# Kernel tuning notes

Measured on AMD Instinct MI355X. Metric: run time of the kernel, lower is better.

The kernel has to match this reference:

```python
import jax, jax.numpy as jnp
import numpy as np

EMBED_DIM = 1024
NUM_HEADS = 16
HEAD_DIM = EMBED_DIM // NUM_HEADS
FF_DIM = 4096
B, T, S = 2, 2048, 2048
LN_EPS = 1e-5


def setup_inputs() -> dict:
    key = jax.random.key(0)
    ks = jax.random.split(key, 20)
    sd = 1.0 / np.sqrt(EMBED_DIM)
    d = {
        'x': jax.random.normal(ks[0], (B, T, EMBED_DIM), jnp.float32),
        'encoder_outputs': jax.random.normal(ks[1], (B, S, EMBED_DIM), jnp.float32),
        'tgt_mask': jnp.tril(jnp.ones((T, T), bool))[None, None],  # [1,1,T,T] causal
    }
    # weights stored [in, out] so y = x @ W + b
    names = ['sa_wq', 'sa_wk', 'sa_wv', 'sa_wo', 'ca_wq', 'ca_wk', 'ca_wv', 'ca_wo']
    for i, n in enumerate(names):
        d[n] = jax.random.normal(ks[2 + i], (EMBED_DIM, EMBED_DIM), jnp.float32) * sd
        d[n.replace('w', 'b')] = jnp.zeros((EMBED_DIM,), jnp.float32)
    d['ff_w1'] = jax.random.normal(ks[10], (EMBED_DIM, FF_DIM), jnp.float32) * sd
    d['ff_b1'] = jnp.zeros((FF_DIM,), jnp.float32)
    d['ff_w2'] = jax.random.normal(ks[11], (FF_DIM, EMBED_DIM), jnp.float32) * (1.0 / np.sqrt(FF_DIM))
    d['ff_b2'] = jnp.zeros((EMBED_DIM,), jnp.float32)
    for i in (1, 2, 3):
        d[f'ln{i}_g'] = jnp.ones((EMBED_DIM,), jnp.float32)
        d[f'ln{i}_b'] = jnp.zeros((EMBED_DIM,), jnp.float32)
    return d


def _layernorm(x, g, b):
    mu = jnp.mean(x, -1, keepdims=True)
    var = jnp.mean(jnp.square(x - mu), -1, keepdims=True)
    return (x - mu) * jax.lax.rsqrt(var + LN_EPS) * g + b


def _mha(q_in, k_in, v_in, wq, bq, wk, bk, wv, bv, wo, bo, mask=None):
    Bq, Tq, C = q_in.shape
    Tk = k_in.shape[1]
    Q = (q_in @ wq + bq).reshape(Bq, Tq, NUM_HEADS, HEAD_DIM)
    K = (k_in @ wk + bk).reshape(Bq, Tk, NUM_HEADS, HEAD_DIM)
    V = (v_in @ wv + bv).reshape(Bq, Tk, NUM_HEADS, HEAD_DIM)
    scores = jnp.einsum('bqhd,bkhd->bhqk', Q, K) / np.sqrt(HEAD_DIM)
    if mask is not None:
        scores = jnp.where(mask, scores, -jnp.inf)
    attn = jax.nn.softmax(scores, axis=-1)
    out = jnp.einsum('bhqk,bkhd->bqhd', attn, V).reshape(Bq, Tq, C)
    return out @ wo + bo


def reference(x, encoder_outputs, tgt_mask,
              sa_wq, sa_bq, sa_wk, sa_bk, sa_wv, sa_bv, sa_wo, sa_bo,
              ca_wq, ca_bq, ca_wk, ca_bk, ca_wv, ca_bv, ca_wo, ca_bo,
              ff_w1, ff_b1, ff_w2, ff_b2,
              ln1_g, ln1_b, ln2_g, ln2_b, ln3_g, ln3_b):
    h = _layernorm(x, ln1_g, ln1_b)
    x = x + _mha(h, h, h, sa_wq, sa_bq, sa_wk, sa_bk, sa_wv, sa_bv, sa_wo, sa_bo, tgt_mask)
    h = _layernorm(x, ln2_g, ln2_b)
    x = x + _mha(h, encoder_outputs, encoder_outputs,
                 ca_wq, ca_bq, ca_wk, ca_bk, ca_wv, ca_bv, ca_wo, ca_bo, None)
    h = _layernorm(x, ln3_g, ln3_b)
    ff = jax.nn.relu(h @ ff_w1 + ff_b1) @ ff_w2 + ff_b2
    return x + ff
```

## Files before the change

### kernel.cpp

```cpp
#include <hip/hip_runtime.h>
#include <stdint.h>


typedef __bf16 bf16x8 __attribute__((ext_vector_type(8)));
typedef float  f32x4  __attribute__((ext_vector_type(4)));

#define T_SEQ 2048
#define NROWS 4096
#define QSCALE 0.18033688011112042f

__device__ __forceinline__ unsigned short f2bf(float f) {
  union { float f; unsigned int u; } v; v.f = f;
  unsigned int u = v.u;
  return (unsigned short)((u + 0x7FFFu + ((u >> 16) & 1u)) >> 16);
}
__device__ __forceinline__ float bf2f(unsigned short h) {
  union { unsigned int u; float f; } v; v.u = ((unsigned int)h) << 16;
  return v.f;
}
__device__ __forceinline__ unsigned int pk2(float a, float b) {
  return (unsigned int)f2bf(a) | ((unsigned int)f2bf(b) << 16);
}
__device__ __forceinline__ unsigned int pk2t(float a, float b) {
  union { float f; unsigned int u; } ua, ub;
  ua.f = a; ub.f = b;
  return __builtin_amdgcn_perm(ub.u, ua.u, 0x07060302u);
}
__device__ __forceinline__ float fexp2(float x) {
  return __builtin_amdgcn_exp2f(x);
}
union U4 { unsigned int u[4]; bf16x8 v; };

__global__ void probe_dtype_kernel(const unsigned short* __restrict__ p,
                                   int* __restrict__ flag) {
  __shared__ int cnt;
  if (threadIdx.x == 0) cnt = 0;
  __syncthreads();
  int bad = 0;
  for (int i = threadIdx.x; i < 4096; i += 256) {
    unsigned short u = p[i];
    int e = (u >> 7) & 0xFF;
    if (u != 0 && (e < 100 || e > 140)) bad++;
  }
  atomicAdd(&cnt, bad);
  __syncthreads();
  if (threadIdx.x == 0) *flag = (cnt < 512) ? 1 : 0;
}

struct WTbl {
  const void* src[10];
  int K[10], N[10], start[10];
  unsigned int dstoff[10];
};
__global__ void wtrans_fused_kernel(WTbl tbl, unsigned short* __restrict__ wsbase,
                                    const int* __restrict__ flag) {
  __shared__ unsigned short tile[32][33];
  const int lb = blockIdx.x;
  int wi = 0;
#pragma unroll
  for (int i = 1; i < 10; i++) wi = (lb >= tbl.start[i]) ? i : wi;
  const int local = lb - tbl.start[wi];
  const int Nw = tbl.N[wi], Kw = tbl.K[wi];
  const int bx = local & ((Nw >> 5) - 1);
  const int by = local / (Nw >> 5);
  const void* W = tbl.src[wi];
  unsigned short* Wt = wsbase + tbl.dstoff[wi];
  const int n0 = bx * 32, k0 = by * 32;
  const int c = threadIdx.x & 31, r0 = threadIdx.x >> 5;
  const bool isbf = (*flag != 0);
  for (int r = r0; r < 32; r += 8) {
    unsigned short v;
    if (isbf) v = ((const unsigned short*)W)[(size_t)(k0 + r) * Nw + n0 + c];
    else      v = f2bf(((const float*)W)[(size_t)(k0 + r) * Nw + n0 + c]);
    tile[r][c] = v;
  }
  __syncthreads();
  const bool packed = (wi == 3) || (wi >= 7);
  if (!packed) {
    for (int r = r0; r < 32; r += 8)
      Wt[(size_t)(n0 + r) * Kw + k0 + c] = tile[c][r];
  } else {
    const int k = k0 + c;
    const size_t kpart = ((size_t)(k >> 5) << 9) + ((((k >> 3) & 3) << 7) + (k & 7));
    const size_t kfr = (size_t)(Kw >> 5);
    for (int r = r0; r < 32; r += 8) {
      const int n = n0 + r;
      Wt[((size_t)(n >> 4) * kfr << 9) + kpart + ((n & 15) << 3)] = tile[c][r];
    }
  }
}

struct PTbl { const void* p[19]; };
__global__ void param_cvt_kernel(PTbl tbl, float* __restrict__ out,
                                 const int* __restrict__ flag) {
  const int blk = blockIdx.x;
  const int off = (blk >= 8 && blk < 12) ? (blk - 8) * 1024 : 0;
  const void* src = tbl.p[blk];
  const int i = threadIdx.x * 4;
  float4 o;
  if (*flag) {
    const unsigned short* u = (const unsigned short*)src + off;
    ushort4 q = *(const ushort4*)&u[i];
    o.x = bf2f(q.x); o.y = bf2f(q.y); o.z = bf2f(q.z); o.w = bf2f(q.w);
  } else {
    o = *(const float4*)&((const float*)src)[off + i];
  }
  *(float4*)&out[blk * 1024 + i] = o;
}

__global__ void cvt_to_bf16_kernel(const void* __restrict__ in,
                                   unsigned short* __restrict__ out,
                                   int n, const int* __restrict__ flag) {
  int i = (blockIdx.x * 256 + threadIdx.x) * 8;
  if (i >= n) return;
  if (*flag) {
    *(int4*)&out[i] = *(const int4*)&((const unsigned short*)in)[i];
  } else {
    const float* f = (const float*)in;
    float4 a = *(const float4*)&f[i];
    float4 c = *(const float4*)&f[i + 4];
    ushort4 o1, o2;
    o1.x = f2bf(a.x); o1.y = f2bf(a.y); o1.z = f2bf(a.z); o1.w = f2bf(a.w);
    o2.x = f2bf(c.x); o2.y = f2bf(c.y); o2.z = f2bf(c.z); o2.w = f2bf(c.w);
    *(ushort4*)&out[i] = o1;
    *(ushort4*)&out[i + 4] = o2;
  }
}

__global__ void cvt_to_f32_kernel(const void* __restrict__ in,
                                  float* __restrict__ out,
                                  int n, const int* __restrict__ flag) {
  int i = (blockIdx.x * 256 + threadIdx.x) * 4;
  if (i >= n) return;
  if (*flag) {
    const unsigned short* u = (const unsigned short*)in;
    ushort4 q = *(const ushort4*)&u[i];
    float4 o;
    o.x = bf2f(q.x); o.y = bf2f(q.y); o.z = bf2f(q.z); o.w = bf2f(q.w);
    *(float4*)&out[i] = o;
  } else {
    *(float4*)&out[i] = *(const float4*)&((const float*)in)[i];
  }
}

__global__ __launch_bounds__(256) void ln_kernel(
    const float* __restrict__ x, const float* __restrict__ g,
    const float* __restrict__ b, unsigned short* __restrict__ out) {
  const int row = blockIdx.x;
  const int t = threadIdx.x;
  const size_t base = (size_t)row * 1024;
  float4 v = *(const float4*)&x[base + t * 4];
  float s1 = v.x + v.y + v.z + v.w;
  float s2 = v.x * v.x + v.y * v.y + v.z * v.z + v.w * v.w;
#pragma unroll
  for (int d = 1; d < 64; d <<= 1) {
    s1 += __shfl_xor(s1, d, 64);
    s2 += __shfl_xor(s2, d, 64);
  }
  __shared__ float a1[4], a2[4];
  if ((t & 63) == 0) { a1[t >> 6] = s1; a2[t >> 6] = s2; }
  __syncthreads();
  s1 = a1[0] + a1[1] + a1[2] + a1[3];
  s2 = a2[0] + a2[1] + a2[2] + a2[3];
  const float mean = s1 * (1.0f / 1024.0f);
  const float var = s2 * (1.0f / 1024.0f) - mean * mean;
  const float rstd = rsqrtf(fmaxf(var, 0.0f) + 1e-5f);
  float4 gv = *(const float4*)&g[t * 4];
  float4 bv = *(const float4*)&b[t * 4];
  ushort4 o;
  o.x = f2bf((v.x - mean) * rstd * gv.x + bv.x);
  o.y = f2bf((v.y - mean) * rstd * gv.y + bv.y);
  o.z = f2bf((v.z - mean) * rstd * gv.z + bv.z);
  o.w = f2bf((v.w - mean) * rstd * gv.w + bv.w);
  *(ushort4*)&out[base + t * 4] = o;
}

template <int BM, int BN, int BK, int RELU, int RESID, int OUTM,
          int BIASROW, int SCALEMODE, int SPLITK>
__global__ __launch_bounds__(256, 2) void gemm_kernel(
    const unsigned short* __restrict__ A, const unsigned short* __restrict__ Bt,
    const float* __restrict__ bias, const float* __restrict__ resid,
    void* __restrict__ outp, int M, int N, int K,
    const int* __restrict__ flag, void* __restrict__ outp2) {
  static_assert(BK == 64, "swizzle assumes 8 chunks/row");
  constexpr int WX = (BN == 64) ? 1 : 2;
  constexpr int WY = 4 / WX;
  constexpr int WM = BM / WY, WN = BN / WX;
  constexpr int MI = WM / 16, NJ = WN / 16;
  constexpr int ACALLS = BM * BK / 2048;
  constexpr int RPC = 2048 / BK;
  __shared__ unsigned short lsA[2][BM * BK];
  const int t = threadIdx.x;
  const int wave = t >> 6, lane = t & 63;
  const int ml = lane & 15, quad = lane >> 4;
  const int cx = ml & 7;
  const int wm = (wave / WX) * WM, wn = (wave % WX) * WN;

  const int nx = gridDim.x, ny = gridDim.y;
  const int lin = (int)blockIdx.y * nx + (int)blockIdx.x;
  const int per = 8 * nx;
  const int y0 = (lin / per) * 8;
  const int gsz = (ny - y0 < 8) ? (ny - y0) : 8;
  const int by = y0 + (lin % gsz);
  const int bx = (lin % per) / gsz;
  const size_t m0 = (size_t)by * BM;
  const size_t n0 = (size_t)bx * BN;

  f32x4 acc[MI][NJ];
  const f32x4 fz = {0.f, 0.f, 0.f, 0.f};
#pragma unroll
  for (int i = 0; i < MI; i++)
#pragma unroll
    for (int j = 0; j < NJ; j++) acc[i][j] = fz;

  const int rowL = t >> 3;
  const int colL = (((t & 7) ^ ((t >> 3) & 7)) * 8);
  const unsigned short* gA = A + (m0 + rowL) * (size_t)K + colL;
  const int kfr = K >> 5;
  const unsigned short* gBp =
      Bt + ((size_t)((n0 + wn) >> 4) * kfr) * 512 + lane * 8;

  auto stageA = [&](unsigned short* dA, int k0) {
#pragma unroll
    for (int c = 0; c < ACALLS; c++)
      __builtin_amdgcn_global_load_lds(
          (const __attribute__((address_space(1))) void*)(gA + (size_t)(c * RPC) * K + k0),
          (__attribute__((address_space(3))) void*)(dA + c * 2048 + wave * 512), 16, 0, 0);
  };
  auto loadB = [&](bf16x8 (&bq)[NJ][2], int k0) {
#pragma unroll
    for (int j = 0; j < NJ; j++)
#pragma unroll
      for (int h = 0; h < 2; h++)
        bq[j][h] = *(const bf16x8*)(gBp + ((size_t)j * kfr + (k0 >> 5) + h) * 512);
  };
  auto comp = [&](const unsigned short* bA, const bf16x8 (&bq)[NJ][2]) {
#pragma unroll
    for (int h = 0; h < 2; h++) {
      bf16x8 af[MI];
#pragma unroll
      for (int i = 0; i < MI; i++)
        af[i] = *(const bf16x8*)
            &bA[(wm + i * 16 + ml) * BK + (((h * 4 + quad) ^ cx) * 8)];
#pragma unroll
      for (int i = 0; i < MI; i++)
#pragma unroll
        for (int j = 0; j < NJ; j++)
          acc[i][j] = __builtin_amdgcn_mfma_f32_16x16x32_bf16(af[i], bq[j][h],
                                                              acc[i][j], 0, 0, 0);
    }
  };

  const int kbase = SPLITK ? (int)blockIdx.z * (K >> 1) : 0;
  const int nk = (SPLITK ? (K >> 1) : K) / BK;
  bf16x8 bq0[NJ][2], bq1[NJ][2];
  stageA(&lsA[0][0], kbase);
  loadB(bq0, kbase);
  int tk = 0;
  while (tk < nk) {
    asm volatile("s_waitcnt vmcnt(0)" ::: "memory");
    __builtin_amdgcn_s_barrier();
    if (tk + 1 < nk) { stageA(&lsA[1][0], kbase + (tk + 1) * BK); loadB(bq1, kbase + (tk + 1) * BK); }
    comp(&lsA[0][0], bq0);
    if (tk + 1 < nk) {
      asm volatile("s_waitcnt vmcnt(0)" ::: "memory");
      __builtin_amdgcn_s_barrier();
      if (tk + 2 < nk) { stageA(&lsA[0][0], kbase + (tk + 2) * BK); loadB(bq0, kbase + (tk + 2) * BK); }
      comp(&lsA[1][0], bq1);
    }
    tk += 2;
  }

  if constexpr (SPLITK) {
    float* po = (blockIdx.z == 0) ? (float*)outp : (float*)outp2;
#pragma unroll
    for (int i = 0; i < MI; i++)
#pragma unroll
      for (int r = 0; r < 4; r++) {
        const size_t rg = m0 + wm + i * 16 + quad * 4 + r;
        float* prow = po + rg * N + n0 + wn + ml;
#pragma unroll
        for (int j = 0; j < NJ; j++) prow[j * 16] = acc[i][j][r];
      }
    return;
  }

  const bool obf = (OUTM == 1) || (OUTM == 2 && *flag != 0);
  float bcol[NJ], scv[NJ];
#pragma unroll
  for (int j = 0; j < NJ; j++) {
    const size_t cg = n0 + wn + j * 16 + ml;
    bcol[j] = BIASROW ? 0.0f : bias[cg];
    scv[j] = (SCALEMODE == 0) ? 1.0f
           : (SCALEMODE == 1) ? QSCALE
                              : (cg < 1024 ? QSCALE : 1.0f);
  }
#pragma unroll
  for (int i = 0; i < MI; i++) {
#pragma unroll
    for (int r = 0; r < 4; r++) {
      const size_t rg = m0 + wm + i * 16 + quad * 4 + r;
      const float brow = BIASROW ? bias[rg] : 0.0f;
      const size_t rbase = rg * N + n0 + wn + ml;
#pragma unroll
      for (int j = 0; j < NJ; j++) {
        float v = (acc[i][j][r] + (BIASROW ? brow : bcol[j])) * scv[j];
        if (RELU) v = fmaxf(v, 0.0f);
        if (RESID) v += resid[rbase + j * 16];
        if (obf) ((unsigned short*)outp)[rbase + j * 16] = f2bf(v);
        else     ((float*)outp)[rbase + j * 16] = v;
      }
    }
  }
}

template <int F32OUT>
__global__ __launch_bounds__(256) void combine_kernel(
    const float* __restrict__ p0, const float* __restrict__ p1,
    const float* __restrict__ bias, const float* __restrict__ resid,
    void* __restrict__ out, const int* __restrict__ flag) {
  const int row = blockIdx.x;
  const int i = threadIdx.x * 4;
  const size_t off = (size_t)row * 1024 + i;
  float4 a = *(const float4*)&p0[off];
  float4 b = *(const float4*)&p1[off];
  float4 r = *(const float4*)&resid[off];
  float4 bb = *(const float4*)&bias[i];
  float4 v;
  v.x = a.x + b.x + bb.x + r.x;
  v.y = a.y + b.y + bb.y + r.y;
  v.z = a.z + b.z + bb.z + r.z;
  v.w = a.w + b.w + bb.w + r.w;
  if (F32OUT || !*flag) {
    *(float4*)&((float*)out)[off] = v;
  } else {
    ushort4 o;
    o.x = f2bf(v.x); o.y = f2bf(v.y); o.z = f2bf(v.z); o.w = f2bf(v.w);
    *(ushort4*)&((unsigned short*)out)[off] = o;
  }
}

struct GSeg {
  const unsigned short* A; const unsigned short* B;
  const float* bias; unsigned short* out;
  int N, K, start, gxlog2, mode;
};
template <int NSEG>
__global__ __launch_bounds__(256, 4) void gemm_multi_kernel(GSeg s0, GSeg s1,
                                                            GSeg s2) {
  constexpr int BM = 128, BN = 64, BK = 64;
  constexpr int WM = 32, WN = 64;
  constexpr int MI = 2, NJ = 4;
  __shared__ unsigned short lsA[BM * BK];
  __shared__ unsigned short lsB[BN * BK];
  const int blk = (int)blockIdx.x;
  GSeg sg = s0;
  if (NSEG > 1 && blk >= s1.start) sg = s1;
  if (NSEG > 2 && blk >= s2.start) sg = s2;
  const int t = threadIdx.x;
  const int wave = t >> 6, lane = t & 63;
  const int ml = lane & 15, quad = lane >> 4;
  const int cx = ml & 7;
  const int wm = wave * WM, wn = 0;
  const int N = sg.N, K = sg.K;

  const int lin = blk - sg.start;
  const int per = 8 << sg.gxlog2;
  const int y0 = (lin / per) * 8;
  const int by = y0 + (lin & 7);
  const int bx = (lin & (per - 1)) >> 3;
  const size_t m0 = (size_t)by * BM;
  const size_t n0 = (size_t)bx * BN;

  f32x4 acc[MI][NJ];
  const f32x4 fz = {0.f, 0.f, 0.f, 0.f};
#pragma unroll
  for (int i = 0; i < MI; i++)
#pragma unroll
    for (int j = 0; j < NJ; j++) acc[i][j] = fz;

  const int rowL = t >> 3;
  const int colL = (((t & 7) ^ ((t >> 3) & 7)) * 8);
  const unsigned short* gA = sg.A + (m0 + rowL) * (size_t)K + colL;
  const unsigned short* gB = sg.B + (n0 + rowL) * (size_t)K + colL;

  for (int k0 = 0; k0 < K; k0 += BK) {
    __syncthreads();
#pragma unroll
    for (int c = 0; c < 4; c++)
      __builtin_amdgcn_global_load_lds(
          (const __attribute__((address_space(1))) void*)(gA + (size_t)(c * 32) * K + k0),
          (__attribute__((address_space(3))) void*)&lsA[c * 2048 + wave * 512], 16, 0, 0);
#pragma unroll
    for (int c = 0; c < 2; c++)
      __builtin_amdgcn_global_load_lds(
          (const __attribute__((address_space(1))) void*)(gB + (size_t)(c * 32) * K + k0),
          (__attribute__((address_space(3))) void*)&lsB[c * 2048 + wave * 512], 16, 0, 0);
    __syncthreads();
#pragma unroll
    for (int h = 0; h < BK / 32; h++) {
      bf16x8 af[MI], bfv[NJ];
#pragma unroll
      for (int i = 0; i < MI; i++)
        af[i] = *(const bf16x8*)
            &lsA[(wm + i * 16 + ml) * BK + (((h * 4 + quad) ^ cx) * 8)];
#pragma unroll
      for (int j = 0; j < NJ; j++)
        bfv[j] = *(const bf16x8*)
            &lsB[(wn + j * 16 + ml) * BK + (((h * 4 + quad) ^ cx) * 8)];
#pragma unroll
      for (int i = 0; i < MI; i++)
#pragma unroll
        for (int j = 0; j < NJ; j++)
          acc[i][j] = __builtin_amdgcn_mfma_f32_16x16x32_bf16(af[i], bfv[j],
                                                              acc[i][j], 0, 0, 0);
    }
  }

  const int mode = sg.mode;
  float bcol[NJ], scv[NJ];
#pragma unroll
  for (int j = 0; j < NJ; j++) {
    const size_t cg = n0 + wn + j * 16 + ml;
    bcol[j] = (mode & 1) ? 0.0f : sg.bias[cg];
    scv[j] = (mode & 2) ? QSCALE
           : ((mode & 4) && cg < 1024) ? QSCALE : 1.0f;
  }
#pragma unroll
  for (int i = 0; i < MI; i++) {
#pragma unroll
    for (int r = 0; r < 4; r++) {
      const size_t rg = m0 + wm + i * 16 + quad * 4 + r;
      const float brow = (mode & 1) ? sg.bias[rg] : 0.0f;
      unsigned short* orow = sg.out + rg * N + n0 + wn + ml;
#pragma unroll
      for (int j = 0; j < NJ; j++) {
        float v = (acc[i][j][r] + ((mode & 1) ? brow : bcol[j])) * scv[j];
        orow[j * 16] = f2bf(v);
      }
    }
  }
}

template <int CAUSAL>
__global__ __launch_bounds__(256, 4) void attn_kernel(
    const unsigned short* __restrict__ Q, const unsigned short* __restrict__ K,
    const unsigned short* __restrict__ VT, unsigned short* __restrict__ O,
    int qstride, int kstride) {
  __shared__ unsigned short Ks[2][4096];
  __shared__ unsigned short Vs[2][4096];
  __shared__ unsigned short Qs[4096];
  const int t = threadIdx.x;
  const int wave = t >> 6, lane = t & 63;
  const int ml = lane & 15, quad = lane >> 4;
  const int cx = ml & 7;
  const int bh = blockIdx.y, b = bh >> 4, h = bh & 15;
  const int px = (((int)blockIdx.x & 3) << 3) | ((int)blockIdx.x >> 2);
  const int qb = CAUSAL ? ((px + (int)blockIdx.y) & 31) : (int)blockIdx.x;
  const int q0 = qb * 64;
  const int lr = lane >> 3;
  const int scol = (((lane & 7) ^ lr) * 8);

  {
    const unsigned short* g0 =
        Q + ((size_t)(b * T_SEQ + q0 + wave * 16 + lr)) * qstride + h * 64 + scol;
    __builtin_amdgcn_global_load_lds(
        (const __attribute__((address_space(1))) void*)g0,
        (__attribute__((address_space(3))) void*)&Qs[wave * 2 * 512], 16, 0, 0);
    const unsigned short* g1 = g0 + (size_t)8 * qstride;
    __builtin_amdgcn_global_load_lds(
        (const __attribute__((address_space(1))) void*)g1,
        (__attribute__((address_space(3))) void*)&Qs[(wave * 2 + 1) * 512], 16, 0, 0);
  }

  int sp_[2];
#pragma unroll
  for (int i = 0; i < 2; i++) {
    int p = (wave * 2 + i) * 8 + lr;
    sp_[i] = ((p & 16) << 1) | ((p & 12) << 1) | ((p & 32) >> 3) | (p & 3);
  }
  const unsigned short* kg0 =
      K + ((size_t)b * T_SEQ + sp_[0]) * kstride + h * 64 + scol;
  const unsigned short* kg1 =
      K + ((size_t)b * T_SEQ + sp_[1]) * kstride + h * 64 + scol;
  const unsigned short* vg0 =
      VT + ((size_t)(h * 64 + wave * 16 + lr)) * 4096 + (size_t)b * T_SEQ + scol;
  const unsigned short* vg1 = vg0 + (size_t)8 * 4096;
  const size_t kinc = (size_t)64 * kstride;

  __syncthreads();
  const bf16x8 aq0 = *(const bf16x8*)&Qs[(wave * 16 + ml) * 64 + ((quad ^ cx) * 8)];
  const bf16x8 aq1 = *(const bf16x8*)&Qs[(wave * 16 + ml) * 64 + (((quad + 4) ^ cx) * 8)];

  f32x4 acc[4];
  const f32x4 fz = {0.f, 0.f, 0.f, 0.f};
#pragma unroll
  for (int n = 0; n < 4; n++) acc[n] = fz;
  float m_i = -3.0e38f, l_part = 0.0f;
  const int q_glob = q0 + wave * 16 + ml;
  const int nkb = CAUSAL ? (qb + 1) : (T_SEQ / 64);

  auto stage = [&](unsigned short* kdst, unsigned short* vdst) {
    __builtin_amdgcn_global_load_lds(
        (const __attribute__((address_space(1))) void*)kg0,
        (__attribute__((address_space(3))) void*)(kdst + (wave * 2) * 512), 16, 0, 0);
    __builtin_amdgcn_global_load_lds(
        (const __attribute__((address_space(1))) void*)kg1,
        (__attribute__((address_space(3))) void*)(kdst + (wave * 2 + 1) * 512), 16, 0, 0);
    __builtin_amdgcn_global_load_lds(
        (const __attribute__((address_space(1))) void*)vg0,
        (__attribute__((address_space(3))) void*)(vdst + (wave * 2) * 512), 16, 0, 0);
    __builtin_amdgcn_global_load_lds(
        (const __attribute__((address_space(1))) void*)vg1,
        (__attribute__((address_space(3))) void*)(vdst + (wave * 2 + 1) * 512), 16, 0, 0);
    kg0 += kinc; kg1 += kinc; vg0 += 64; vg1 += 64;
  };

  auto compute = [&](const unsigned short* Kb, const unsigned short* Vb, int kb) {
    f32x4 s[4];
#pragma unroll
    for (int nt = 0; nt < 4; nt++) {
      bf16x8 k0 = *(const bf16x8*)&Kb[(nt * 16 + ml) * 64 + ((quad ^ cx) * 8)];
      bf16x8 k1 = *(const bf16x8*)&Kb[(nt * 16 + ml) * 64 + (((quad + 4) ^ cx) * 8)];
      f32x4 a = fz;
      a = __builtin_amdgcn_mfma_f32_16x16x32_bf16(k0, aq0, a, 0, 0, 0);
      a = __builtin_amdgcn_mfma_f32_16x16x32_bf16(k1, aq1, a, 0, 0, 0);
      s[nt] = a;
    }
    if (CAUSAL && kb == nkb - 1) {
#pragma unroll
      for (int nt = 0; nt < 4; nt++)
#pragma unroll
        for (int r = 0; r < 4; r++) {
          int key = kb * 64 + ((nt & 1) << 5) + (quad << 3) + ((nt >> 1) << 2) + r;
          if (key > q_glob) s[nt][r] = -3.0e38f;
        }
    }
    float tm = -3.0e38f;
#pragma unroll
    for (int nt = 0; nt < 4; nt++)
#pragma unroll
      for (int r = 0; r < 4; r++) tm = fmaxf(tm, s[nt][r]);
    tm = fmaxf(tm, __shfl_xor(tm, 16));
    tm = fmaxf(tm, __shfl_xor(tm, 32));
    if (__any(tm > m_i + 8.0f)) {
      const float m_new = fmaxf(m_i, tm);
      const float alpha = fexp2(m_i - m_new);
      l_part *= alpha;
#pragma unroll
      for (int n = 0; n < 4; n++)
#pragma unroll
        for (int r = 0; r < 4; r++) acc[n][r] *= alpha;
      m_i = m_new;
    }
    float p[4][4];
    float rs = 0.f;
#pragma unroll
    for (int nt = 0; nt < 4; nt++)
#pragma unroll
      for (int r = 0; r < 4; r++) {
        p[nt][r] = fexp2(s[nt][r] - m_i);
        rs += p[nt][r];
      }
    l_part += rs;

    U4 P0, P1;
    P0.u[0] = pk2t(p[0][0], p[0][1]); P0.u[1] = pk2t(p[0][2], p[0][3]);
    P0.u[2] = pk2t(p[2][0], p[2][1]); P0.u[3] = pk2t(p[2][2], p[2][3]);
    P1.u[0] = pk2t(p[1][0], p[1][1]); P1.u[1] = pk2t(p[1][2], p[1][3]);
    P1.u[2] = pk2t(p[3][0], p[3][1]); P1.u[3] = pk2t(p[3][2], p[3][3]);

#pragma unroll
    for (int n = 0; n < 4; n++) {
      bf16x8 v0 = *(const bf16x8*)&Vb[(n * 16 + ml) * 64 + ((quad ^ cx) * 8)];
      bf16x8 v1 = *(const bf16x8*)&Vb[(n * 16 + ml) * 64 + (((quad + 4) ^ cx) * 8)];
      acc[n] = __builtin_amdgcn_mfma_f32_16x16x32_bf16(v0, P0.v, acc[n], 0, 0, 0);
      acc[n] = __builtin_amdgcn_mfma_f32_16x16x32_bf16(v1, P1.v, acc[n], 0, 0, 0);
    }
  };

  stage(&Ks[0][0], &Vs[0][0]);
  for (int kb = 0; kb < nkb; kb += 2) {
    asm volatile("s_waitcnt vmcnt(0)" ::: "memory");
    __syncthreads();
    if (kb + 1 < nkb) stage(&Ks[1][0], &Vs[1][0]);
    compute(&Ks[0][0], &Vs[0][0], kb);
    if (kb + 1 < nkb) {
      asm volatile("s_waitcnt vmcnt(0)" ::: "memory");
      __syncthreads();
      if (kb + 2 < nkb) stage(&Ks[0][0], &Vs[0][0]);
      compute(&Ks[1][0], &Vs[1][0], kb + 1);
    }
  }

  float l_i = l_part;
  l_i += __shfl_xor(l_i, 16);
  l_i += __shfl_xor(l_i, 32);

  __syncthreads();
  unsigned short* eps = &Ks[0][0];
  const float inv = 1.0f / l_i;
#pragma unroll
  for (int n = 0; n < 4; n++)
#pragma unroll
    for (int rp = 0; rp < 2; rp++) {
      unsigned int u = pk2(acc[n][2 * rp] * inv, acc[n][2 * rp + 1] * inv);
      *(unsigned int*)&eps[(wave * 16 + ml) * 72 + n * 16 + quad * 4 + 2 * rp] = u;
    }
  __syncthreads();
  {
    const int q = t >> 2, d0 = (t & 3) * 16;
    unsigned short* og = O + ((size_t)(b * T_SEQ + q0 + q)) * 1024 + h * 64 + d0;
    *(int4*)og = *(const int4*)&eps[q * 72 + d0];
    *(int4*)(og + 8) = *(const int4*)&eps[q * 72 + d0 + 8];
  }
}

extern "C" void kernel_launch(void* const* d_in, const int* in_sizes, int n_in,
                              void* d_out, int out_size, void* d_ws,
                              size_t ws_size, hipStream_t stream) {
  (void)in_sizes; (void)n_in; (void)out_size; (void)ws_size;
  const size_t MEG = 1048576;
  unsigned short* ws16 = (unsigned short*)d_ws;
  char* wsb = (char*)d_ws;

  unsigned short* wt[10];
  for (int i = 0; i < 8; i++) wt[i] = ws16 + (size_t)i * MEG;
  wt[8] = ws16 + 8 * MEG;
  wt[9] = ws16 + 12 * MEG;
  unsigned short* encB  = ws16 + 16 * MEG;
  unsigned short* hbuf  = ws16 + 20 * MEG;
  unsigned short* QKb   = ws16 + 24 * MEG;
  unsigned short* Qb    = ws16 + 32 * MEG;
  unsigned short* Kb    = ws16 + 36 * MEG;
  unsigned short* Vb    = ws16 + 40 * MEG;
  unsigned short* attnb = ws16 + 44 * MEG;
  unsigned short* ffh   = ws16 + 24 * MEG;
  float* xf32 = (float*)(wsb + 96 * MEG);
  float* pbuf = (float*)(wsb + 112 * MEG);
  int* flag   = (int*)(wsb + 113 * MEG);
  float* part0 = (float*)(wsb + 32 * MEG);
  float* part1 = (float*)(wsb + 80 * MEG);

  probe_dtype_kernel<<<1, 256, 0, stream>>>((const unsigned short*)d_in[0], flag);

  {
    WTbl tb;
    const int widx[10] = {3, 5, 7, 9, 11, 13, 15, 17, 19, 21};
    int st = 0;
    for (int i = 0; i < 10; i++) {
      tb.src[i] = d_in[widx[i]];
      tb.K[i] = (i == 9) ? 4096 : 1024;
      tb.N[i] = (i == 8) ? 4096 : 1024;
      tb.start[i] = st;
      st += (tb.K[i] / 32) * (tb.N[i] / 32);
      tb.dstoff[i] = (unsigned int)((i < 8) ? i * MEG : (i == 8 ? 8 * MEG : 12 * MEG));
    }
    wtrans_fused_kernel<<<16384, 256, 0, stream>>>(tb, ws16, flag);
  }

  cvt_to_f32_kernel<<<4096, 256, 0, stream>>>(d_in[0], xf32, 4194304, flag);
  cvt_to_bf16_kernel<<<2048, 256, 0, stream>>>(d_in[1], encB, 4194304, flag);

  {
    PTbl pt;
    const int pidx[19] = {4, 6, 8, 10, 12, 14, 16, 18,
                          20, 20, 20, 20, 22, 23, 24, 25, 26, 27, 28};
    for (int i = 0; i < 19; i++) pt.p[i] = d_in[pidx[i]];
    param_cvt_kernel<<<19, 256, 0, stream>>>(pt, pbuf, flag);
  }
  float* bqk_sa = pbuf;
  float* bv_sa  = pbuf + 2048;
  float* bo_sa  = pbuf + 3072;
  float* bq_ca  = pbuf + 4096;
  float* bk_ca  = pbuf + 5120;
  float* bv_ca  = pbuf + 6144;
  float* bo_ca  = pbuf + 7168;
  float* ff_b1p = pbuf + 8192;
  float* ff_b2p = pbuf + 12288;
  float* ln1g = pbuf + 13312; float* ln1b = pbuf + 14336;
  float* ln2g = pbuf + 15360; float* ln2b = pbuf + 16384;
  float* ln3g = pbuf + 17408; float* ln3b = pbuf + 18432;

  dim3 gP(16, 32);
  dim3 gFF1(32, 32);
  dim3 gFF2(8, 64, 2);
  dim3 gAttn(32, 32);

  ln_kernel<<<4096, 256, 0, stream>>>(xf32, ln1g, ln1b, hbuf);
  {
    GSeg sQK = {hbuf, wt[0], bqk_sa, QKb, 2048, 1024, 0, 5, 4};
    GSeg sVT = {wt[2], hbuf, bv_sa, Vb, 4096, 1024, 1024, 6, 1};
    gemm_multi_kernel<2><<<1536, 256, 0, stream>>>(sQK, sVT, sVT);
  }
  attn_kernel<1><<<gAttn, 256, 0, stream>>>(QKb, QKb + 1024, Vb, attnb, 2048, 2048);
  gemm_kernel<128, 64, 64, 0, 1, 0, 0, 0, 0><<<gP, 256, 0, stream>>>(
      attnb, wt[3], bo_sa, xf32, xf32, NROWS, 1024, 1024, nullptr, nullptr);

  ln_kernel<<<4096, 256, 0, stream>>>(xf32, ln2g, ln2b, hbuf);
  {
    GSeg sQ = {hbuf, wt[4], bq_ca, Qb, 1024, 1024, 0, 4, 2};
    GSeg sK = {encB, wt[5], bk_ca, Kb, 1024, 1024, 512, 4, 0};
    GSeg sV = {wt[6], encB, bv_ca, Vb, 4096, 1024, 1024, 6, 1};
    gemm_multi_kernel<3><<<1536, 256, 0, stream>>>(sQ, sK, sV);
  }
  attn_kernel<0><<<gAttn, 256, 0, stream>>>(Qb, Kb, Vb, attnb, 1024, 1024);
  gemm_kernel<128, 64, 64, 0, 1, 0, 0, 0, 0><<<gP, 256, 0, stream>>>(
      attnb, wt[7], bo_ca, xf32, xf32, NROWS, 1024, 1024, nullptr, nullptr);

  ln_kernel<<<4096, 256, 0, stream>>>(xf32, ln3g, ln3b, hbuf);
  gemm_kernel<128, 128, 64, 1, 0, 1, 0, 0, 0><<<gFF1, 256, 0, stream>>>(
      hbuf, wt[8], ff_b1p, nullptr, ffh, NROWS, 4096, 1024, nullptr, nullptr);
  gemm_kernel<64, 128, 64, 0, 0, 0, 0, 0, 1><<<gFF2, 256, 0, stream>>>(
      ffh, wt[9], nullptr, nullptr, part0, NROWS, 1024, 4096, flag, part1);
  combine_kernel<0><<<4096, 256, 0, stream>>>(part0, part1, ff_b2p, xf32,
                                              d_out, flag);
}
```

Before: 553.9 us.

## Single-buffer attention K/V tiles and load Q directly to raise occupancy

The attention kernel drops double-buffered K/V staging and the Q LDS tile, shrinking shared memory from 40KB to 16KB per block. Launch bounds go from 4 to 8 blocks per CU so more blocks can hide latency instead of relying on software prefetch. Q fragments are now read straight from global memory into registers. The cost is that each iteration waits on its own loads with no overlap inside a block, and the epilogue staging buffer (64x72 shorts) must fit in the 8192-short array.

```diff
diff --git a/kernel.cpp b/kernel.cpp
--- a/kernel.cpp
+++ b/kernel.cpp
@@ -443,13 +443,13 @@
 }
 
 template <int CAUSAL>
-__global__ __launch_bounds__(256, 4) void attn_kernel(
+__global__ __launch_bounds__(256, 8) void attn_kernel(
     const unsigned short* __restrict__ Q, const unsigned short* __restrict__ K,
     const unsigned short* __restrict__ VT, unsigned short* __restrict__ O,
     int qstride, int kstride) {
-  __shared__ unsigned short Ks[2][4096];
-  __shared__ unsigned short Vs[2][4096];
-  __shared__ unsigned short Qs[4096];
+  __shared__ unsigned short KVs[8192];
+  unsigned short* Ks = &KVs[0];
+  unsigned short* Vs = &KVs[4096];
   const int t = threadIdx.x;
   const int wave = t >> 6, lane = t & 63;
   const int ml = lane & 15, quad = lane >> 4;
@@ -461,17 +461,10 @@
   const int lr = lane >> 3;
   const int scol = (((lane & 7) ^ lr) * 8);
 
-  {
-    const unsigned short* g0 =
-        Q + ((size_t)(b * T_SEQ + q0 + wave * 16 + lr)) * qstride + h * 64 + scol;
-    __builtin_amdgcn_global_load_lds(
-        (const __attribute__((address_space(1))) void*)g0,
-        (__attribute__((address_space(3))) void*)&Qs[wave * 2 * 512], 16, 0, 0);
-    const unsigned short* g1 = g0 + (size_t)8 * qstride;
-    __builtin_amdgcn_global_load_lds(
-        (const __attribute__((address_space(1))) void*)g1,
-        (__attribute__((address_space(3))) void*)&Qs[(wave * 2 + 1) * 512], 16, 0, 0);
-  }
+  const unsigned short* qrow =
+      Q + ((size_t)(b * T_SEQ + q0 + wave * 16 + ml)) * qstride + h * 64;
+  const bf16x8 aq0 = *(const bf16x8*)(qrow + quad * 8);
+  const bf16x8 aq1 = *(const bf16x8*)(qrow + (quad + 4) * 8);
 
   int sp_[2];
 #pragma unroll
@@ -488,10 +481,6 @@
   const unsigned short* vg1 = vg0 + (size_t)8 * 4096;
   const size_t kinc = (size_t)64 * kstride;
 
-  __syncthreads();
-  const bf16x8 aq0 = *(const bf16x8*)&Qs[(wave * 16 + ml) * 64 + ((quad ^ cx) * 8)];
-  const bf16x8 aq1 = *(const bf16x8*)&Qs[(wave * 16 + ml) * 64 + (((quad + 4) ^ cx) * 8)];
-
   f32x4 acc[4];
   const f32x4 fz = {0.f, 0.f, 0.f, 0.f};
 #pragma unroll
@@ -500,28 +489,29 @@
   const int q_glob = q0 + wave * 16 + ml;
   const int nkb = CAUSAL ? (qb + 1) : (T_SEQ / 64);
 
-  auto stage = [&](unsigned short* kdst, unsigned short* vdst) {
+  for (int kb = 0; kb < nkb; kb++) {
+    __syncthreads();
     __builtin_amdgcn_global_load_lds(
         (const __attribute__((address_space(1))) void*)kg0,
-        (__attribute__((address_space(3))) void*)(kdst + (wave * 2) * 512), 16, 0, 0);
+        (__attribute__((address_space(3))) void*)(Ks + (wave * 2) * 512), 16, 0, 0);
     __builtin_amdgcn_global_load_lds(
         (const __attribute__((address_space(1))) void*)kg1,
-        (__attribute__((address_space(3))) void*)(kdst + (wave * 2 + 1) * 512), 16, 0, 0);
+        (__attribute__((address_space(3))) void*)(Ks + (wave * 2 + 1) * 512), 16, 0, 0);
     __builtin_amdgcn_global_load_lds(
         (const __attribute__((address_space(1))) void*)vg0,
-        (__attribute__((address_space(3))) void*)(vdst + (wave * 2) * 512), 16, 0, 0);
+        (__attribute__((address_space(3))) void*)(Vs + (wave * 2) * 512), 16, 0, 0);
     __builtin_amdgcn_global_load_lds(
         (const __attribute__((address_space(1))) void*)vg1,
-        (__attribute__((address_space(3))) void*)(vdst + (wave * 2 + 1) * 512), 16, 0, 0);
+        (__attribute__((address_space(3))) void*)(Vs + (wave * 2 + 1) * 512), 16, 0, 0);
     kg0 += kinc; kg1 += kinc; vg0 += 64; vg1 += 64;
-  };
-
-  auto compute = [&](const unsigned short* Kb, const unsigned short* Vb, int kb) {
+    asm volatile("s_waitcnt vmcnt(0)" ::: "memory");
+    __syncthreads();
+
     f32x4 s[4];
 #pragma unroll
     for (int nt = 0; nt < 4; nt++) {
-      bf16x8 k0 = *(const bf16x8*)&Kb[(nt * 16 + ml) * 64 + ((quad ^ cx) * 8)];
-      bf16x8 k1 = *(const bf16x8*)&Kb[(nt * 16 + ml) * 64 + (((quad + 4) ^ cx) * 8)];
+      bf16x8 k0 = *(const bf16x8*)&Ks[(nt * 16 + ml) * 64 + ((quad ^ cx) * 8)];
+      bf16x8 k1 = *(const bf16x8*)&Ks[(nt * 16 + ml) * 64 + (((quad + 4) ^ cx) * 8)];
       f32x4 a = fz;
       a = __builtin_amdgcn_mfma_f32_16x16x32_bf16(k0, aq0, a, 0, 0, 0);
       a = __builtin_amdgcn_mfma_f32_16x16x32_bf16(k1, aq1, a, 0, 0, 0);
@@ -572,24 +562,10 @@
 
 #pragma unroll
     for (int n = 0; n < 4; n++) {
-      bf16x8 v0 = *(const bf16x8*)&Vb[(n * 16 + ml) * 64 + ((quad ^ cx) * 8)];
-      bf16x8 v1 = *(const bf16x8*)&Vb[(n * 16 + ml) * 64 + (((quad + 4) ^ cx) * 8)];
+      bf16x8 v0 = *(const bf16x8*)&Vs[(n * 16 + ml) * 64 + ((quad ^ cx) * 8)];
+      bf16x8 v1 = *(const bf16x8*)&Vs[(n * 16 + ml) * 64 + (((quad + 4) ^ cx) * 8)];
       acc[n] = __builtin_amdgcn_mfma_f32_16x16x32_bf16(v0, P0.v, acc[n], 0, 0, 0);
       acc[n] = __builtin_amdgcn_mfma_f32_16x16x32_bf16(v1, P1.v, acc[n], 0, 0, 0);
-    }
-  };
-
-  stage(&Ks[0][0], &Vs[0][0]);
-  for (int kb = 0; kb < nkb; kb += 2) {
-    asm volatile("s_waitcnt vmcnt(0)" ::: "memory");
-    __syncthreads();
-    if (kb + 1 < nkb) stage(&Ks[1][0], &Vs[1][0]);
-    compute(&Ks[0][0], &Vs[0][0], kb);
-    if (kb + 1 < nkb) {
-      asm volatile("s_waitcnt vmcnt(0)" ::: "memory");
-      __syncthreads();
-      if (kb + 2 < nkb) stage(&Ks[0][0], &Vs[0][0]);
-      compute(&Ks[1][0], &Vs[1][0], kb + 1);
     }
   }
 
@@ -598,7 +574,7 @@
   l_i += __shfl_xor(l_i, 32);
 
   __syncthreads();
-  unsigned short* eps = &Ks[0][0];
+  unsigned short* eps = &KVs[0];
   const float inv = 1.0f / l_i;
 #pragma unroll
   for (int n = 0; n < 4; n++)
```

New measurement: 564.6 us. No clear change (+1.9%).
